# Optimization experiments

Measured on AMD Instinct MI355X. Metric: run time of the kernel, lower is better.

## Reference

```python
import jax, jax.numpy as jnp
import numpy as np

N_EMBD = 1024
HEAD_SIZE = 64
WINDOW = 64
N_GLOBAL = 64
N_RANDOM = 64
B, T = 8, 2048


def setup_inputs() -> dict:
    key = jax.random.key(0)
    kx, kc, kk, kq, kv = jax.random.split(key, 5)
    x = jax.random.normal(kx, (B, T, N_EMBD), dtype=jnp.float32)
    random_cols = jax.random.randint(kc, (T, N_RANDOM), 0, T)
    s = 1.0 / np.sqrt(N_EMBD)
    Wk = jax.random.normal(kk, (HEAD_SIZE, N_EMBD), dtype=jnp.float32) * s
    Wq = jax.random.normal(kq, (HEAD_SIZE, N_EMBD), dtype=jnp.float32) * s
    Wv = jax.random.normal(kv, (HEAD_SIZE, N_EMBD), dtype=jnp.float32) * s
    return {"x": x, "random_cols": random_cols, "Wk": Wk, "Wq": Wq, "Wv": Wv}


def _bigbird_mask(Tlen, random_cols):
    rows = jnp.arange(Tlen)[:, None]
    cols = jnp.arange(Tlen)[None, :]
    causal = rows >= cols
    local = (cols >= rows - WINDOW + 1) & (cols <= rows)
    glob = (rows < N_GLOBAL) | (cols < N_GLOBAL)
    rand = jnp.zeros((Tlen, Tlen), dtype=bool).at[
        jnp.arange(Tlen)[:, None], random_cols].set(True)
    return (local | glob | rand) & causal  # [T, T] bool


def reference(x, random_cols, Wk, Wq, Wv):
    # projections (Linear, no bias): [B,T,C] @ [C,H] -> [B,T,H]
    k = jnp.einsum('btc,hc->bth', x, Wk)
    q = jnp.einsum('btc,hc->bth', x, Wq)
    v = jnp.einsum('btc,hc->bth', x, Wv)
    scale = 1.0 / jnp.sqrt(jnp.asarray(HEAD_SIZE, x.dtype))
    scores = jnp.einsum('bqh,bkh->bqk', q, k) * scale  # [B,T,T]
    mask = _bigbird_mask(x.shape[1], random_cols)
    scores = jnp.where(mask[None, :, :], scores, -jnp.inf)
    weights = jax.nn.softmax(scores, axis=-1)
    out = jnp.einsum('bqk,bkh->bqh', weights, v)  # [B,T,H]
    return out
```

## Files before the change

kernel.cpp:

```cpp
#include <hip/hip_runtime.h>
#include <math.h>

#define T_DIM 2048
#define C_DIM 1024
#define H_DIM 64
#define M_TOTAL 16384
#define NQKV 192

typedef __bf16 bf16x8 __attribute__((ext_vector_type(8)));
typedef float f32x4 __attribute__((ext_vector_type(4)));
typedef float f32x2 __attribute__((ext_vector_type(2)));
typedef unsigned short u16x8 __attribute__((ext_vector_type(8)));

#if __has_builtin(__builtin_amdgcn_fdot2_f32_bf16)
#define HAVE_DOT2 1
typedef __bf16 bf16x2 __attribute__((ext_vector_type(2)));
#else
#define HAVE_DOT2 0
#endif

__device__ __forceinline__ unsigned short f2bf(float f) {
    unsigned u = __float_as_uint(f);
    unsigned r = (u + 0x7FFFu + ((u >> 16) & 1u)) >> 16;
    return (unsigned short)r;
}
__device__ __forceinline__ float bf2f(unsigned short u) {
    return __uint_as_float(((unsigned)u) << 16);
}
__device__ __forceinline__ float blo(unsigned u) { return __uint_as_float(u << 16); }
__device__ __forceinline__ float bhi(unsigned u) { return __uint_as_float(u & 0xFFFF0000u); }
__device__ __forceinline__ unsigned pack_bf2(float f0, float f1) {
    unsigned u0 = __float_as_uint(f0) + 0x8000u;
    unsigned u1 = __float_as_uint(f1) + 0x8000u;
    return __builtin_amdgcn_perm(u1, u0, 0x07060302u);
}
__device__ __forceinline__ uint4 cvt8(float4 a, float4 b) {
    return make_uint4(pack_bf2(a.x, a.y), pack_bf2(a.z, a.w),
                      pack_bf2(b.x, b.y), pack_bf2(b.z, b.w));
}

__device__ __forceinline__ float dot8bf(u16x8 a, u16x8 b, float c) {
#if HAVE_DOT2
    bf16x8 av = __builtin_bit_cast(bf16x8, a);
    bf16x8 bv = __builtin_bit_cast(bf16x8, b);
    #pragma unroll
    for (int e = 0; e < 4; ++e) {
        bf16x2 ap = {av[2 * e], av[2 * e + 1]};
        bf16x2 bp = {bv[2 * e], bv[2 * e + 1]};
        c = __builtin_amdgcn_fdot2_f32_bf16(ap, bp, c, false);
    }
#else
    #pragma unroll
    for (int e = 0; e < 8; ++e) c = fmaf(bf2f(a[e]), bf2f(b[e]), c);
#endif
    return c;
}

__global__ __launch_bounds__(512) void proj_kernel(
    const float* __restrict__ x,
    const float* __restrict__ Wk,
    const float* __restrict__ Wq,
    const float* __restrict__ Wv,
    unsigned short* __restrict__ qkv)
{
    __shared__ unsigned short Ab[64 * 64];
    __shared__ unsigned short Bb[192 * 64];

    const int m0 = blockIdx.x * 64;
    const int t  = threadIdx.x;
    const int wv = t >> 6, ln = t & 63;
    const int mfr = ln & 15, kq = ln >> 4;
    const int r0 = (wv & 1) * 32;
    const int c0 = (wv >> 1) * 48;

    const int srow  = t >> 3;
    const int sk8   = (t & 7) * 8;
    const int skoff = sk8 ^ ((srow & 7) * 8);

    const float* gp[4] = {
        x  + (size_t)(m0 + srow) * C_DIM + sk8,
        Wk + (size_t)srow * C_DIM + sk8,
        Wq + (size_t)srow * C_DIM + sk8,
        Wv + (size_t)srow * C_DIM + sk8 };
    unsigned short* lp[4] = {
        &Ab[srow * 64 + skoff],
        &Bb[srow * 64 + skoff],
        &Bb[(srow + 64) * 64 + skoff],
        &Bb[(srow + 128) * 64 + skoff] };

    f32x4 acc[2][3] = {};

    float4 ra[4], rb[4];
    #pragma unroll
    for (int s = 0; s < 4; ++s) {
        ra[s] = *(const float4*)(gp[s]);
        rb[s] = *(const float4*)(gp[s] + 4);
    }

    for (int kc = 0; kc < C_DIM; kc += 64) {
        __syncthreads();
        #pragma unroll
        for (int s = 0; s < 4; ++s)
            *(uint4*)lp[s] = cvt8(ra[s], rb[s]);
        if (kc + 64 < C_DIM) {
            #pragma unroll
            for (int s = 0; s < 4; ++s) {
                ra[s] = *(const float4*)(gp[s] + kc + 64);
                rb[s] = *(const float4*)(gp[s] + kc + 68);
            }
        }
        __syncthreads();
        #pragma unroll
        for (int ks = 0; ks < 64; ks += 32) {
            bf16x8 af[2], bf[3];
            #pragma unroll
            for (int a = 0; a < 2; ++a) {
                int row = r0 + a * 16 + mfr;
                af[a] = *(const bf16x8*)&Ab[row * 64 + ((ks + kq * 8) ^ ((row & 7) * 8))];
            }
            #pragma unroll
            for (int b2 = 0; b2 < 3; ++b2) {
                int row = c0 + b2 * 16 + mfr;
                bf[b2] = *(const bf16x8*)&Bb[row * 64 + ((ks + kq * 8) ^ ((row & 7) * 8))];
            }
            #pragma unroll
            for (int a = 0; a < 2; ++a)
                #pragma unroll
                for (int b2 = 0; b2 < 3; ++b2)
                    acc[a][b2] = __builtin_amdgcn_mfma_f32_16x16x32_bf16(
                        af[a], bf[b2], acc[a][b2], 0, 0, 0);
        }
    }

    #pragma unroll
    for (int a = 0; a < 2; ++a)
        #pragma unroll
        for (int b2 = 0; b2 < 3; ++b2)
            #pragma unroll
            for (int r = 0; r < 4; ++r) {
                int row = m0 + r0 + a * 16 + kq * 4 + r;
                int col = c0 + b2 * 16 + mfr;
                qkv[(size_t)row * NQKV + col] = f2bf(acc[a][b2][r]);
            }
}

__global__ __launch_bounds__(256) void attn_kernel(
    const unsigned short* __restrict__ qkv,
    const int*  __restrict__ rnd,
    float* __restrict__ out)
{
    const int wv = threadIdx.x >> 6;
    const int ln = threadIdx.x & 63;
    const int b  = blockIdx.x & 7;
    const int i  = ((blockIdx.x >> 3) << 2) + wv;
    const int bi = b * T_DIM + i;

    __shared__ float    wt_all[4][192];
    __shared__ int      rj_all[4][64];
    __shared__ unsigned bm_all[4][64];
    float*    wt = wt_all[wv];
    int*      rj = rj_all[wv];
    unsigned* bm = bm_all[wv];

    bm[ln] = 0u;
    rj[ln] = 0;

    bool v0 = (ln <= i);
    bool v1 = (ln < i - 63);
    int  j2 = rnd[i * 64 + ln];
    bool v2 = (j2 < i - 63) && (j2 >= 64);
    if (v2) {
        unsigned old = atomicOr(&bm[j2 >> 5], 1u << (j2 & 31));
        v2 = ((old >> (j2 & 31)) & 1u) == 0u;
    }
    unsigned long long mbal = __ballot(v2);
    const int nval = __popcll(mbal);
    if (v2) {
        int pos = __popcll(mbal & ((1ull << ln) - 1ull));
        rj[pos] = j2;
    }

    const int e8 = (ln & 7) * 8;
    const int gg = ln >> 3;
    u16x8 qraw = *(const u16x8*)(qkv + (size_t)bi * NQKV + 64 + e8);

    const unsigned short* kb = qkv + (size_t)b * T_DIM * NQKV;

    #pragma unroll
    for (int n = 0; n < 16; n += 4) {
        int jj[4];
        #pragma unroll
        for (int u = 0; u < 4; ++u) {
            int s = (n + u) * 8 + gg;
            int j;
            if (s < 64) { j = i - s; j = (j < 0) ? 0 : j; }
            else        { j = s - 64; }
            jj[u] = j;
        }
        u16x8 kv[4];
        #pragma unroll
        for (int u = 0; u < 4; ++u)
            kv[u] = *(const u16x8*)(kb + (size_t)jj[u] * NQKV + e8);
        #pragma unroll
        for (int u = 0; u < 4; ++u) {
            float p = dot8bf(kv[u], qraw, 0.f);
            p += __shfl_xor(p, 1);
            p += __shfl_xor(p, 2);
            p += __shfl_xor(p, 4);
            if ((ln & 7) == 0) wt[(n + u) * 8 + gg] = p;
        }
    }

    auto qk_rand = [&](int n0) {
        int jj[4];
        #pragma unroll
        for (int u = 0; u < 4; ++u) jj[u] = rj[(n0 - 16 + u) * 8 + gg];
        u16x8 kv[4];
        #pragma unroll
        for (int u = 0; u < 4; ++u)
            kv[u] = *(const u16x8*)(kb + (size_t)jj[u] * NQKV + e8);
        #pragma unroll
        for (int u = 0; u < 4; ++u) {
            float p = dot8bf(kv[u], qraw, 0.f);
            p += __shfl_xor(p, 1);
            p += __shfl_xor(p, 2);
            p += __shfl_xor(p, 4);
            if ((ln & 7) == 0) wt[(n0 + u) * 8 + gg] = p;
        }
    };
    if (nval > 0)  qk_rand(16);
    if (nval > 32) qk_rand(20);

    const bool vs2 = (ln < nval);
    float s0 = wt[ln];
    float s1 = wt[64 + ln];
    float s2 = vs2 ? wt[128 + ln] : 0.f;
    s0 = v0  ? s0 * 0.125f : -1e30f;
    s1 = v1  ? s1 * 0.125f : -1e30f;
    s2 = vs2 ? s2 * 0.125f : -1e30f;

    float mx = fmaxf(s0, fmaxf(s1, s2));
    #pragma unroll
    for (int m = 32; m; m >>= 1) mx = fmaxf(mx, __shfl_xor(mx, m));
    float e0 = v0  ? __expf(s0 - mx) : 0.f;
    float e1 = v1  ? __expf(s1 - mx) : 0.f;
    float e2 = vs2 ? __expf(s2 - mx) : 0.f;
    float sum = e0 + e1 + e2;
    #pragma unroll
    for (int m = 32; m; m >>= 1) sum += __shfl_xor(sum, m);

    wt[ln]       = e0;
    wt[64 + ln]  = e1;
    wt[128 + ln] = e2;

    const unsigned short* vb = kb + 128;
    f32x2 acc2[4] = {};
    #pragma unroll
    for (int bt = 0; bt < 2; ++bt) {
        float w[8]; int jc[8];
        #pragma unroll
        for (int c = 0; c < 8; ++c) {
            int s = (bt * 8 + c) * 8 + gg;
            w[c] = wt[s];
            int j;
            if (s < 64) { j = i - s; j = (j < 0) ? 0 : j; }
            else        { j = s - 64; }
            jc[c] = j;
        }
        uint4 vv[8];
        #pragma unroll
        for (int c = 0; c < 8; ++c)
            vv[c] = *(const uint4*)(vb + (size_t)jc[c] * NQKV + e8);
        #pragma unroll
        for (int c = 0; c < 8; ++c) {
            f32x2 w2 = {w[c], w[c]};
            f32x2 p0 = {blo(vv[c].x), bhi(vv[c].x)};
            f32x2 p1 = {blo(vv[c].y), bhi(vv[c].y)};
            f32x2 p2 = {blo(vv[c].z), bhi(vv[c].z)};
            f32x2 p3 = {blo(vv[c].w), bhi(vv[c].w)};
            acc2[0] += w2 * p0;
            acc2[1] += w2 * p1;
            acc2[2] += w2 * p2;
            acc2[3] += w2 * p3;
        }
    }
    auto pv_rand = [&](int c0) {
        float w[4]; int jc[4];
        #pragma unroll
        for (int c = 0; c < 4; ++c) {
            int ridx = (c0 + c) * 8 + gg;
            w[c]  = wt[128 + ridx];
            jc[c] = rj[ridx];
        }
        uint4 vv[4];
        #pragma unroll
        for (int c = 0; c < 4; ++c)
            vv[c] = *(const uint4*)(vb + (size_t)jc[c] * NQKV + e8);
        #pragma unroll
        for (int c = 0; c < 4; ++c) {
            f32x2 w2 = {w[c], w[c]};
            f32x2 p0 = {blo(vv[c].x), bhi(vv[c].x)};
            f32x2 p1 = {blo(vv[c].y), bhi(vv[c].y)};
            f32x2 p2 = {blo(vv[c].z), bhi(vv[c].z)};
            f32x2 p3 = {blo(vv[c].w), bhi(vv[c].w)};
            acc2[0] += w2 * p0;
            acc2[1] += w2 * p1;
            acc2[2] += w2 * p2;
            acc2[3] += w2 * p3;
        }
    };
    if (nval > 0)  pv_rand(0);
    if (nval > 32) pv_rand(4);

    float acc[8] = { acc2[0][0], acc2[0][1], acc2[1][0], acc2[1][1],
                     acc2[2][0], acc2[2][1], acc2[3][0], acc2[3][1] };
    #pragma unroll
    for (int m = 8; m <= 32; m <<= 1)
        #pragma unroll
        for (int e = 0; e < 8; ++e)
            acc[e] += __shfl_xor(acc[e], m);

    if (ln < 8) {
        float inv = 1.f / sum;
        float* op = &out[(size_t)bi * H_DIM + e8];
        *(float4*)op       = make_float4(acc[0]*inv, acc[1]*inv, acc[2]*inv, acc[3]*inv);
        *(float4*)(op + 4) = make_float4(acc[4]*inv, acc[5]*inv, acc[6]*inv, acc[7]*inv);
    }
}

extern "C" void kernel_launch(void* const* d_in, const int* in_sizes, int n_in,
                              void* d_out, int out_size, void* d_ws, size_t ws_size,
                              hipStream_t stream) {
    const float* x   = (const float*)d_in[0];
    const int*   rnd = (const int*)  d_in[1];
    const float* Wk  = (const float*)d_in[2];
    const float* Wq  = (const float*)d_in[3];
    const float* Wv  = (const float*)d_in[4];
    float* out = (float*)d_out;
    unsigned short* qkv = (unsigned short*)d_ws;

    proj_kernel<<<M_TOTAL / 64, 512, 0, stream>>>(x, Wk, Wq, Wv, qkv);
    attn_kernel<<<M_TOTAL / 4, 256, 0, stream>>>(qkv, rnd, out);
}
```

Before: 148.8 us.

## Precompute random-column compaction once, use DPP reductions, remap PV lanes

Moves the per-row dedup and compaction of random columns into a separate kernel. It runs once per query row instead of once per batch and row, so attention reads the compacted indices and counts from workspace. It replaces the shfl_xor reductions in QK and softmax with DPP row operations and writes four scores per lane group with one select. The PV loop is remapped so each lane handles a contiguous 8-element slice of the head dimension, with vectorized weight and index loads, and the final reduction stays within 8 lanes. The cost is an extra kernel launch and a workspace offset that assumes enough space after qkv.

```diff
diff --git a/kernel.cpp b/kernel.cpp
--- a/kernel.cpp
+++ b/kernel.cpp
@@ -54,6 +54,80 @@
     for (int e = 0; e < 8; ++e) c = fmaf(bf2f(a[e]), bf2f(b[e]), c);
 #endif
     return c;
+}
+
+#if __has_builtin(__builtin_amdgcn_update_dpp)
+#define HAVE_DPP 1
+template<int CTRL>
+__device__ __forceinline__ float dppf(float x) {
+    int v = __builtin_amdgcn_update_dpp(0, __builtin_bit_cast(int, x),
+                                        CTRL, 0xF, 0xF, true);
+    return __builtin_bit_cast(float, v);
+}
+__device__ __forceinline__ float red8(float p) {
+    p += dppf<0xB1>(p);
+    p += dppf<0x4E>(p);
+    p += dppf<0x141>(p);
+    return p;
+}
+__device__ __forceinline__ float redsum16(float p) {
+    p += dppf<0xB1>(p);
+    p += dppf<0x4E>(p);
+    p += dppf<0x141>(p);
+    p += dppf<0x140>(p);
+    return p;
+}
+__device__ __forceinline__ float redmax16(float p) {
+    p = fmaxf(p, dppf<0xB1>(p));
+    p = fmaxf(p, dppf<0x4E>(p));
+    p = fmaxf(p, dppf<0x141>(p));
+    p = fmaxf(p, dppf<0x140>(p));
+    return p;
+}
+#else
+#define HAVE_DPP 0
+__device__ __forceinline__ float red8(float p) {
+    p += __shfl_xor(p, 1); p += __shfl_xor(p, 2); p += __shfl_xor(p, 4);
+    return p;
+}
+__device__ __forceinline__ float redsum16(float p) {
+    p += __shfl_xor(p, 1); p += __shfl_xor(p, 2);
+    p += __shfl_xor(p, 4); p += __shfl_xor(p, 8);
+    return p;
+}
+__device__ __forceinline__ float redmax16(float p) {
+    p = fmaxf(p, __shfl_xor(p, 1)); p = fmaxf(p, __shfl_xor(p, 2));
+    p = fmaxf(p, __shfl_xor(p, 4)); p = fmaxf(p, __shfl_xor(p, 8));
+    return p;
+}
+#endif
+
+__global__ __launch_bounds__(256) void compact_kernel(
+    const int* __restrict__ rnd,
+    int* __restrict__ rjc,
+    int* __restrict__ nvalb)
+{
+    __shared__ unsigned bm_all[4][64];
+    const int wv = threadIdx.x >> 6;
+    const int ln = threadIdx.x & 63;
+    const int i  = blockIdx.x * 4 + wv;
+    unsigned* bm = bm_all[wv];
+
+    bm[ln] = 0u;
+    int  j2 = rnd[i * 64 + ln];
+    bool v2 = (j2 < i - 63) && (j2 >= 64);
+    if (v2) {
+        unsigned old = atomicOr(&bm[j2 >> 5], 1u << (j2 & 31));
+        v2 = ((old >> (j2 & 31)) & 1u) == 0u;
+    }
+    unsigned long long mbal = __ballot(v2);
+    const int nval = __popcll(mbal);
+    if (v2) {
+        int pos = __popcll(mbal & ((1ull << ln) - 1ull));
+        rjc[i * 64 + pos] = j2;
+    }
+    if (ln >= nval) rjc[i * 64 + ln] = 0;
+    if (ln == 0) nvalb[i] = nval;
 }
 
 __global__ __launch_bounds__(512) void proj_kernel(
@@ -146,7 +220,8 @@
 
 __global__ __launch_bounds__(256) void attn_kernel(
     const unsigned short* __restrict__ qkv,
-    const int*  __restrict__ rnd,
+    const int*  __restrict__ rjc,
+    const int*  __restrict__ nvalb,
     float* __restrict__ out)
 {
     const int wv = threadIdx.x >> 6;
@@ -155,35 +230,19 @@
     const int i  = ((blockIdx.x >> 3) << 2) + wv;
     const int bi = b * T_DIM + i;
 
-    __shared__ float    wt_all[4][192];
-    __shared__ int      rj_all[4][64];
-    __shared__ unsigned bm_all[4][64];
-    float*    wt = wt_all[wv];
-    int*      rj = rj_all[wv];
-    unsigned* bm = bm_all[wv];
-
-    bm[ln] = 0u;
-    rj[ln] = 0;
-
-    bool v0 = (ln <= i);
-    bool v1 = (ln < i - 63);
-    int  j2 = rnd[i * 64 + ln];
-    bool v2 = (j2 < i - 63) && (j2 >= 64);
-    if (v2) {
-        unsigned old = atomicOr(&bm[j2 >> 5], 1u << (j2 & 31));
-        v2 = ((old >> (j2 & 31)) & 1u) == 0u;
-    }
-    unsigned long long mbal = __ballot(v2);
-    const int nval = __popcll(mbal);
-    if (v2) {
-        int pos = __popcll(mbal & ((1ull << ln) - 1ull));
-        rj[pos] = j2;
-    }
-
-    const int e8 = (ln & 7) * 8;
-    const int gg = ln >> 3;
-    u16x8 qraw = *(const u16x8*)(qkv + (size_t)bi * NQKV + 64 + e8);
-
+    __shared__ float wt_all[4][192];
+    float* wt = wt_all[wv];
+
+    const int  nval = nvalb[i];
+    const int* rji  = rjc + i * 64;
+
+    const bool v0 = (ln <= i);
+    const bool v1 = (ln < i - 63);
+
+    const int e8q = (ln & 7) * 8;
+    const int gg  = ln >> 3;
+    const int lq  = ln & 7;
+    u16x8 qraw = *(const u16x8*)(qkv + (size_t)bi * NQKV + 64 + e8q);
     const unsigned short* kb = qkv + (size_t)b * T_DIM * NQKV;
 
     #pragma unroll
@@ -200,33 +259,31 @@
         u16x8 kv[4];
         #pragma unroll
         for (int u = 0; u < 4; ++u)
-            kv[u] = *(const u16x8*)(kb + (size_t)jj[u] * NQKV + e8);
-        #pragma unroll
-        for (int u = 0; u < 4; ++u) {
-            float p = dot8bf(kv[u], qraw, 0.f);
-            p += __shfl_xor(p, 1);
-            p += __shfl_xor(p, 2);
-            p += __shfl_xor(p, 4);
-            if ((ln & 7) == 0) wt[(n + u) * 8 + gg] = p;
-        }
+            kv[u] = *(const u16x8*)(kb + (size_t)jj[u] * NQKV + e8q);
+        float p[4];
+        #pragma unroll
+        for (int u = 0; u < 4; ++u)
+            p[u] = red8(dot8bf(kv[u], qraw, 0.f));
+        float pw = (lq & 2) ? ((lq & 1) ? p[3] : p[2])
+                            : ((lq & 1) ? p[1] : p[0]);
+        if (lq < 4) wt[(n + lq) * 8 + gg] = pw;
     }
 
     auto qk_rand = [&](int n0) {
         int jj[4];
         #pragma unroll
-        for (int u = 0; u < 4; ++u) jj[u] = rj[(n0 - 16 + u) * 8 + gg];
+        for (int u = 0; u < 4; ++u) jj[u] = rji[(n0 - 16 + u) * 8 + gg];
         u16x8 kv[4];
         #pragma unroll
         for (int u = 0; u < 4; ++u)
-            kv[u] = *(const u16x8*)(kb + (size_t)jj[u] * NQKV + e8);
-        #pragma unroll
-        for (int u = 0; u < 4; ++u) {
-            float p = dot8bf(kv[u], qraw, 0.f);
-            p += __shfl_xor(p, 1);
-            p += __shfl_xor(p, 2);
-            p += __shfl_xor(p, 4);
-            if ((ln & 7) == 0) wt[(n0 + u) * 8 + gg] = p;
-        }
+            kv[u] = *(const u16x8*)(kb + (size_t)jj[u] * NQKV + e8q);
+        float p[4];
+        #pragma unroll
+        for (int u = 0; u < 4; ++u)
+            p[u] = red8(dot8bf(kv[u], qraw, 0.f));
+        float pw = (lq & 2) ? ((lq & 1) ? p[3] : p[2])
+                            : ((lq & 1) ? p[1] : p[0]);
+        if (lq < 4) wt[(n0 + lq) * 8 + gg] = pw;
     };
     if (nval > 0)  qk_rand(16);
     if (nval > 32) qk_rand(20);
@@ -240,40 +297,45 @@
     s2 = vs2 ? s2 * 0.125f : -1e30f;
 
     float mx = fmaxf(s0, fmaxf(s1, s2));
-    #pragma unroll
-    for (int m = 32; m; m >>= 1) mx = fmaxf(mx, __shfl_xor(mx, m));
+    mx = redmax16(mx);
+    mx = fmaxf(mx, __shfl_xor(mx, 16));
+    mx = fmaxf(mx, __shfl_xor(mx, 32));
     float e0 = v0  ? __expf(s0 - mx) : 0.f;
     float e1 = v1  ? __expf(s1 - mx) : 0.f;
     float e2 = vs2 ? __expf(s2 - mx) : 0.f;
     float sum = e0 + e1 + e2;
-    #pragma unroll
-    for (int m = 32; m; m >>= 1) sum += __shfl_xor(sum, m);
+    sum = redsum16(sum);
+    sum += __shfl_xor(sum, 16);
+    sum += __shfl_xor(sum, 32);
 
     wt[ln]       = e0;
     wt[64 + ln]  = e1;
     wt[128 + ln] = e2;
 
+    const int gp  = ln & 7;
+    const int ee8 = (ln >> 3) * 8;
     const unsigned short* vb = kb + 128;
     f32x2 acc2[4] = {};
-    #pragma unroll
-    for (int bt = 0; bt < 2; ++bt) {
-        float w[8]; int jc[8];
-        #pragma unroll
-        for (int c = 0; c < 8; ++c) {
-            int s = (bt * 8 + c) * 8 + gg;
-            w[c] = wt[s];
+
+    #pragma unroll
+    for (int bt = 0; bt < 4; ++bt) {
+        f32x4 w4 = *(const f32x4*)&wt[bt * 32 + gp * 4];
+        int jc[4];
+        #pragma unroll
+        for (int c = 0; c < 4; ++c) {
+            int s = bt * 32 + gp * 4 + c;
             int j;
             if (s < 64) { j = i - s; j = (j < 0) ? 0 : j; }
             else        { j = s - 64; }
             jc[c] = j;
         }
-        uint4 vv[8];
-        #pragma unroll
-        for (int c = 0; c < 8; ++c)
-            vv[c] = *(const uint4*)(vb + (size_t)jc[c] * NQKV + e8);
-        #pragma unroll
-        for (int c = 0; c < 8; ++c) {
-            f32x2 w2 = {w[c], w[c]};
+        uint4 vv[4];
+        #pragma unroll
+        for (int c = 0; c < 4; ++c)
+            vv[c] = *(const uint4*)(vb + (size_t)jc[c] * NQKV + ee8);
+        #pragma unroll
+        for (int c = 0; c < 4; ++c) {
+            f32x2 w2 = {w4[c], w4[c]};
             f32x2 p0 = {blo(vv[c].x), bhi(vv[c].x)};
             f32x2 p1 = {blo(vv[c].y), bhi(vv[c].y)};
             f32x2 p2 = {blo(vv[c].z), bhi(vv[c].z)};
@@ -284,21 +346,18 @@
             acc2[3] += w2 * p3;
         }
     }
-    auto pv_rand = [&](int c0) {
-        float w[4]; int jc[4];
+
+    auto pv_rand = [&](int r0) {
+        int4  j4 = *(const int4*)&rji[r0 + gp * 4];
+        f32x4 w4 = *(const f32x4*)&wt[128 + r0 + gp * 4];
+        int jc[4] = { j4.x, j4.y, j4.z, j4.w };
+        uint4 vv[4];
+        #pragma unroll
+        for (int c = 0; c < 4; ++c)
+            vv[c] = *(const uint4*)(vb + (size_t)jc[c] * NQKV + ee8);
         #pragma unroll
         for (int c = 0; c < 4; ++c) {
-            int ridx = (c0 + c) * 8 + gg;
-            w[c]  = wt[128 + ridx];
-            jc[c] = rj[ridx];
-        }
-        uint4 vv[4];
-        #pragma unroll
-        for (int c = 0; c < 4; ++c)
-            vv[c] = *(const uint4*)(vb + (size_t)jc[c] * NQKV + e8);
-        #pragma unroll
-        for (int c = 0; c < 4; ++c) {
-            f32x2 w2 = {w[c], w[c]};
+            f32x2 w2 = {w4[c], w4[c]};
             f32x2 p0 = {blo(vv[c].x), bhi(vv[c].x)};
             f32x2 p1 = {blo(vv[c].y), bhi(vv[c].y)};
             f32x2 p2 = {blo(vv[c].z), bhi(vv[c].z)};
@@ -310,19 +369,28 @@
         }
     };
     if (nval > 0)  pv_rand(0);
-    if (nval > 32) pv_rand(4);
+    if (nval > 32) pv_rand(32);
 
     float acc[8] = { acc2[0][0], acc2[0][1], acc2[1][0], acc2[1][1],
                      acc2[2][0], acc2[2][1], acc2[3][0], acc2[3][1] };
-    #pragma unroll
-    for (int m = 8; m <= 32; m <<= 1)
+#if HAVE_DPP
+    #pragma unroll
+    for (int e = 0; e < 8; ++e) {
+        acc[e] += dppf<0xB1>(acc[e]);
+        acc[e] += dppf<0x4E>(acc[e]);
+        acc[e] += dppf<0x141>(acc[e]);
+    }
+#else
+    #pragma unroll
+    for (int m = 1; m <= 4; m <<= 1)
         #pragma unroll
         for (int e = 0; e < 8; ++e)
             acc[e] += __shfl_xor(acc[e], m);
-
-    if (ln < 8) {
+#endif
+
+    if (gp == 0) {
         float inv = 1.f / sum;
-        float* op = &out[(size_t)bi * H_DIM + e8];
+        float* op = &out[(size_t)bi * H_DIM + ee8];
         *(float4*)op       = make_float4(acc[0]*inv, acc[1]*inv, acc[2]*inv, acc[3]*inv);
         *(float4*)(op + 4) = make_float4(acc[4]*inv, acc[5]*inv, acc[6]*inv, acc[7]*inv);
     }
@@ -337,8 +405,12 @@
     const float* Wq  = (const float*)d_in[3];
     const float* Wv  = (const float*)d_in[4];
     float* out = (float*)d_out;
+
     unsigned short* qkv = (unsigned short*)d_ws;
-
+    int* rjc   = (int*)((char*)d_ws + 6291456);
+    int* nvalb = rjc + T_DIM * 64;
+
+    compact_kernel<<<T_DIM / 4, 256, 0, stream>>>(rnd, rjc, nvalb);
     proj_kernel<<<M_TOTAL / 64, 512, 0, stream>>>(x, Wk, Wq, Wv, qkv);
-    attn_kernel<<<M_TOTAL / 4, 256, 0, stream>>>(qkv, rnd, out);
-}
+    attn_kernel<<<M_TOTAL / 4, 256, 0, stream>>>(qkv, rjc, nvalb, out);
+}
```

New measurement: 172.4 us. 15.9% more time.
